# Kernel optimization log

Measured on AMD Instinct MI355X. Metric: run time of the kernel, lower is better.

The kernel has to match this reference:

```python
import jax, jax.numpy as jnp
import numpy as np

N_HEAD = 16
ROPE_BASE = 10000.0


def _make_rope(max_seq, half_dim):
    inv_freq = 1.0 / (ROPE_BASE ** (np.arange(0, half_dim, dtype=np.float32) / half_dim))
    t = np.arange(max_seq, dtype=np.float32)
    freqs = np.outer(t, inv_freq)  # [T, half_dim]
    return jnp.asarray(np.cos(freqs)), jnp.asarray(np.sin(freqs))


def setup_inputs() -> dict:
    key = jax.random.key(0)
    k1, k2, k3 = jax.random.split(key, 3)
    B, T, C = 4, 2048, 2048
    D = C // N_HEAD
    x = jax.random.normal(k1, (B, T, C), dtype=jnp.float32)
    # torch Linear weight [out,in]; stored transposed so y = x @ W
    wqkv = jax.random.normal(k2, (C, 3 * C), dtype=jnp.float32) * (C ** -0.5)
    wo = jax.random.normal(k3, (C, C), dtype=jnp.float32) * (C ** -0.5)
    rope_cos, rope_sin = _make_rope(T, D // 2)
    return {"x": x, "wqkv": wqkv, "wo": wo, "rope_cos": rope_cos, "rope_sin": rope_sin}


def _apply_rope(t, cos, sin):
    # t: [B, T, H, D]; cos/sin: [T, D/2]
    B, T, H, D = t.shape
    tr = t.reshape(B, T, H, D // 2, 2)
    xr, xi = tr[..., 0], tr[..., 1]
    c = cos[:T][None, :, None, :]
    s = sin[:T][None, :, None, :]
    out_r = xr * c - xi * s
    out_i = xr * s + xi * c
    return jnp.stack([out_r, out_i], axis=-1).reshape(B, T, H, D)


def reference(x, wqkv, wo, rope_cos, rope_sin):
    B, T, C = x.shape
    H = N_HEAD
    D = C // H
    qkv = x @ wqkv  # [B, T, 3C]
    q, k, v = jnp.split(qkv, 3, axis=-1)
    q = _apply_rope(q.reshape(B, T, H, D), rope_cos, rope_sin)
    k = _apply_rope(k.reshape(B, T, H, D), rope_cos, rope_sin)
    v = v.reshape(B, T, H, D)
    scale = D ** -0.5
    scores = jnp.einsum('bqhd,bkhd->bhqk', q, k) * scale  # [B, H, T, T]
    causal = jnp.tril(jnp.ones((T, T), dtype=bool))
    scores = jnp.where(causal[None, None], scores, jnp.finfo(scores.dtype).min)
    attn = jax.nn.softmax(scores, axis=-1)
    y = jnp.einsum('bhqk,bkhd->bqhd', attn, v).reshape(B, T, C)
    return y @ wo
```

## Files before the change

### kernel.cpp

```cpp
#include <hip/hip_runtime.h>
#include <hip/hip_bf16.h>

typedef __attribute__((ext_vector_type(8))) __bf16 bf16x8;
typedef __attribute__((ext_vector_type(4))) float f32x4;
typedef __attribute__((ext_vector_type(4))) unsigned short us4;

__device__ __forceinline__ unsigned short f2bf(float f) {
    unsigned u = __float_as_uint(f);
    u += 0x7FFFu + ((u >> 16) & 1u);
    return (unsigned short)(u >> 16);
}

__device__ __forceinline__ void gload16(const void* g, void* l) {
    __builtin_amdgcn_global_load_lds(
        (const __attribute__((address_space(1))) unsigned int*)g,
        (__attribute__((address_space(3))) unsigned int*)l,
        16, 0, 0);
}

__global__ void cvt_f32_bf16(const float* __restrict__ in, unsigned short* __restrict__ out, int n4) {
    int i = blockIdx.x * blockDim.x + threadIdx.x;
    if (i >= n4) return;
    float4 v = ((const float4*)in)[i];
    us4 r = { f2bf(v.x), f2bf(v.y), f2bf(v.z), f2bf(v.w) };
    ((us4*)out)[i] = r;
}

__global__ void tcvt(const float* __restrict__ in, unsigned short* __restrict__ out, int R, int C) {
    __shared__ float tile[32][33];
    int tx = threadIdx.x & 31, ty = threadIdx.x >> 5;
    int c0 = blockIdx.x * 32, r0 = blockIdx.y * 32;
    #pragma unroll
    for (int i = 0; i < 32; i += 8)
        tile[ty + i][tx] = in[(size_t)(r0 + ty + i) * C + c0 + tx];
    __syncthreads();
    #pragma unroll
    for (int i = 0; i < 32; i += 8)
        out[(size_t)(c0 + ty + i) * R + r0 + tx] = f2bf(tile[tx][ty + i]);
}

#define MFW(af, bf, fi, ni) acc[fi][ni] = __builtin_amdgcn_mfma_f32_16x16x32_bf16(af, bf, acc[fi][ni], 0, 0, 0)
#define MFMA16W() do { \
    MFW(a0,b0,0,0); MFW(a0,b1,0,1); MFW(a0,b2,0,2); MFW(a0,b3,0,3); \
    MFW(a1,b0,1,0); MFW(a1,b1,1,1); MFW(a1,b2,1,2); MFW(a1,b3,1,3); \
    MFW(a2,b0,2,0); MFW(a2,b1,2,1); MFW(a2,b2,2,2); MFW(a2,b3,2,3); \
    MFW(a3,b0,3,0); MFW(a3,b1,3,1); MFW(a3,b2,3,2); MFW(a3,b3,3,3); } while(0)
#define STGW(kt, bufo) do { \
    size_t ko = (size_t)(kt) * 128; \
    char* bb = L + (bufo); \
    gload16(Ag + sR + ko, bb + dstA); \
    gload16(Ag + sR2 + ko, bb + dstA + 16384); \
    gload16(Bg + sR + ko, bb + 32768 + dstA); \
    gload16(Bg + sR2 + ko, bb + 32768 + dstA + 16384); } while (0)

template <int MODE>
__global__ __launch_bounds__(1024, 4) void gemmw(
    const unsigned short* __restrict__ A, const unsigned short* __restrict__ Bt,
    int M, int N, int K, float* __restrict__ Cf,
    unsigned short* __restrict__ qp, unsigned short* __restrict__ kp,
    unsigned short* __restrict__ vTp,
    const float* __restrict__ ropeC, const float* __restrict__ ropeS,
    int cby, int cbx)
{
    __shared__ unsigned short lds[2][32768];
    const int tid = threadIdx.x;
    const int lane = tid & 63, wid = tid >> 6;
    const int ln15 = lane & 15, hig = lane >> 4;
    const int wrow = wid >> 2, wcol = wid & 3;

    int nwg = gridDim.x * gridDim.y;
    int flat = blockIdx.y * gridDim.x + blockIdx.x;
    int bx, by;
    if ((nwg & 7) == 0) {
        int c = flat & 7, local = flat >> 3;
        int chunkCols = gridDim.x / cbx;
        by = (c / chunkCols) * cby + local / cbx;
        bx = (c % chunkCols) * cbx + local % cbx;
    } else {
        bx = flat % gridDim.x; by = flat / gridDim.x;
    }
    const int mbase = by * 256, nbase = bx * 256;
    const size_t Kb = (size_t)K * 2;

    const char* Ag = (const char*)A + (size_t)mbase * Kb;
    const char* Bg = (const char*)Bt + (size_t)nbase * Kb;
    char* L = (char*)&lds[0][0];

    const int srow = tid >> 3;
    const int gs = (tid & 7) ^ (srow & 7);
    const size_t sR = (size_t)srow * Kb + gs * 16;
    const size_t sR2 = sR + (size_t)128 * Kb;
    const int dstA = tid * 16;

    const int aBase = (wrow * 64 + ln15) * 128;
    const int bBase = 32768 + (wcol * 64 + ln15) * 128;
    const int sl0 = (hig ^ (ln15 & 7)) * 16;
    const int sl1 = ((4 + hig) ^ (ln15 & 7)) * 16;

    f32x4 acc[4][4] = {};
    const int T = K >> 6;

    STGW(0, 0);
    asm volatile("s_waitcnt vmcnt(0)" ::: "memory");
    __builtin_amdgcn_s_barrier();
    asm volatile("" ::: "memory");

    for (int t = 0; t < T; t++) {
        char* bb = L + (t & 1) * 65536;
        if (t + 1 < T) STGW(t + 1, ((t + 1) & 1) * 65536);
        bf16x8 a0, a1, a2, a3, b0, b1, b2, b3;
        a0 = *(const bf16x8*)(bb + aBase + 0 * 2048 + sl0);
        a1 = *(const bf16x8*)(bb + aBase + 1 * 2048 + sl0);
        a2 = *(const bf16x8*)(bb + aBase + 2 * 2048 + sl0);
        a3 = *(const bf16x8*)(bb + aBase + 3 * 2048 + sl0);
        b0 = *(const bf16x8*)(bb + bBase + 0 * 2048 + sl0);
        b1 = *(const bf16x8*)(bb + bBase + 1 * 2048 + sl0);
        b2 = *(const bf16x8*)(bb + bBase + 2 * 2048 + sl0);
        b3 = *(const bf16x8*)(bb + bBase + 3 * 2048 + sl0);
        MFMA16W();
        a0 = *(const bf16x8*)(bb + aBase + 0 * 2048 + sl1);
        a1 = *(const bf16x8*)(bb + aBase + 1 * 2048 + sl1);
        a2 = *(const bf16x8*)(bb + aBase + 2 * 2048 + sl1);
        a3 = *(const bf16x8*)(bb + aBase + 3 * 2048 + sl1);
        b0 = *(const bf16x8*)(bb + bBase + 0 * 2048 + sl1);
        b1 = *(const bf16x8*)(bb + bBase + 1 * 2048 + sl1);
        b2 = *(const bf16x8*)(bb + bBase + 2 * 2048 + sl1);
        b3 = *(const bf16x8*)(bb + bBase + 3 * 2048 + sl1);
        MFMA16W();

        if (t + 1 < T) {
            asm volatile("s_waitcnt vmcnt(0)" ::: "memory");
            __builtin_amdgcn_s_barrier();
            asm volatile("" ::: "memory");
        }
    }

    if (MODE == 0) {
        #pragma unroll
        for (int fm = 0; fm < 4; fm++)
            #pragma unroll
            for (int fn = 0; fn < 4; fn++)
                #pragma unroll
                for (int j = 0; j < 4; j++) {
                    int m = mbase + wrow * 64 + fm * 16 + hig * 4 + j;
                    int col = nbase + wcol * 64 + fn * 16 + ln15;
                    Cf[(size_t)m * N + col] = acc[fm][fn][j];
                }
    } else {
        const int colb = nbase + wcol * 64;
        const int sec = colb >> 11;
        if (sec < 2) {
            unsigned short* dst = (sec == 0) ? qp : kp;
            const float scale = (sec == 0) ? 0.08838834764831845f : 1.0f;
            #pragma unroll
            for (int fm = 0; fm < 4; fm++)
                #pragma unroll
                for (int fn = 0; fn < 4; fn++) {
                    int within = (colb & 2047) + fn * 16 + ln15;
                    int h = within >> 7, d = within & 127, pidx = d >> 1;
                    #pragma unroll
                    for (int j = 0; j < 4; j++) {
                        int m = mbase + wrow * 64 + fm * 16 + hig * 4 + j;
                        int b = m >> 11, tq = m & 2047;
                        float v = acc[fm][fn][j];
                        float pv = __shfl_xor(v, 1);
                        float c = ropeC[tq * 64 + pidx], s = ropeS[tq * 64 + pidx];
                        float o = (d & 1) ? fmaf(pv, s, v * c) : fmaf(-pv, s, v * c);
                        o *= scale;
                        dst[((size_t)((b << 4) + h) * 2048 + tq) * 128 + d] = f2bf(o);
                    }
                }
        } else {
            #pragma unroll
            for (int fm = 0; fm < 4; fm++)
                #pragma unroll
                for (int fn = 0; fn < 4; fn++) {
                    int within = (colb & 2047) + fn * 16 + ln15;
                    int h = within >> 7, d = within & 127;
                    int m0 = mbase + wrow * 64 + fm * 16 + hig * 4;
                    int b = m0 >> 11, t0 = m0 & 2047;
                    us4 pk = { f2bf(acc[fm][fn][0]), f2bf(acc[fm][fn][1]),
                               f2bf(acc[fm][fn][2]), f2bf(acc[fm][fn][3]) };
                    *(us4*)(vTp + ((size_t)((b << 4) + h) * 128 + d) * 2048 + t0) = pk;
                }
        }
    }
}

__global__ __launch_bounds__(256, 2) void attn_fwd(
    const unsigned short* __restrict__ q, const unsigned short* __restrict__ k,
    const unsigned short* __restrict__ vT, unsigned short* __restrict__ outp)
{
    __shared__ unsigned short lK[2][64 * 128];
    __shared__ unsigned short lV[2][128 * 64];
    __shared__ unsigned short lP[4 * 32 * 64];
    const int tid = threadIdx.x;
    const int lane = tid & 63, wid = tid >> 6;
    const int ln15 = lane & 15, hig = lane >> 4, hi8 = hig * 8;
    const int bh = blockIdx.x;

    const char* qg = (const char*)(q + (size_t)bh * 2048 * 128);
    const char* kg = (const char*)(k + (size_t)bh * 2048 * 128);
    const char* vg = (const char*)(vT + (size_t)bh * 128 * 2048);
    char* lKc = (char*)&lK[0][0];
    char* lVc = (char*)&lV[0][0];
    char* lPc = (char*)lP + wid * (32 * 64 * 2);
    const int b = bh >> 4, h = bh & 15;

    for (int rep = 0; rep < 2; rep++) {
        const int qt = rep == 0 ? (int)blockIdx.y : 15 - (int)blockIdx.y;
        const int qbase = qt * 128;
        const int qw = qbase + wid * 32;

        bf16x8 qf[2][4];
        #pragma unroll
        for (int mt = 0; mt < 2; mt++)
            #pragma unroll
            for (int ks = 0; ks < 4; ks++)
                qf[mt][ks] = *(const bf16x8*)(qg + ((size_t)(qw + mt * 16 + ln15) * 128 + ks * 32 + hi8) * 2);

        f32x4 o[2][8] = {};
        float mreg[2] = { -1e30f, -1e30f };
        float lreg[2] = { 0.f, 0.f };

        auto stageKV = [&](int bf, int kv0) {
            #pragma unroll
            for (int i = 0; i < 4; i++) {
                int slot = tid + i * 256;
                int row = slot >> 4, c = (slot & 15) * 16;
                gload16(kg + (size_t)(kv0 + row) * 256 + (c ^ ((row & 7) << 4)),
                        lKc + bf * 16384 + slot * 16);
            }
            #pragma unroll
            for (int i = 0; i < 4; i++) {
                int slot = tid + i * 256;
                int d = slot >> 3, c = (slot & 7) * 16;
                gload16(vg + (size_t)d * 4096 + (size_t)kv0 * 2 + (c ^ ((d & 7) << 4)),
                        lVc + bf * 16384 + slot * 16);
            }
        };

        const int ntiles = (qbase >> 6) + 2;
        stageKV(0, 0);
        if (ntiles > 1) stageKV(1, 64);

        for (int it = 0; it < ntiles; it++) {
            const int kv0 = it * 64;
            const int buf = it & 1;
            if (it + 1 < ntiles) asm volatile("s_waitcnt vmcnt(8)" ::: "memory");
            else                 asm volatile("s_waitcnt vmcnt(0)" ::: "memory");
            __builtin_amdgcn_s_barrier();

            if (kv0 <= qw + 31) {
                const char* lKb = lKc + buf * 16384;
                const char* lVb = lVc + buf * 16384;

                f32x4 s[2][4] = {};
                #pragma unroll
                for (int ks = 0; ks < 4; ks++) {
                    bf16x8 kf[4];
                    #pragma unroll
                    for (int nt = 0; nt < 4; nt++) {
                        int row = nt * 16 + ln15;
                        kf[nt] = *(const bf16x8*)(lKb + row * 256 + (((ks * 32 + hi8) * 2) ^ ((row & 7) << 4)));
                    }
                    __builtin_amdgcn_s_setprio(1);
                    #pragma unroll
                    for (int mt = 0; mt < 2; mt++)
                        #pragma unroll
                        for (int nt = 0; nt < 4; nt++)
                            s[mt][nt] = __builtin_amdgcn_mfma_f32_16x16x32_bf16(kf[nt], qf[mt][ks], s[mt][nt], 0, 0, 0);
                    __builtin_amdgcn_s_setprio(0);
                }

                if (kv0 + 63 > qw) {
                    #pragma unroll
                    for (int mt = 0; mt < 2; mt++) {
                        int qi = qw + mt * 16 + ln15;
                        #pragma unroll
                        for (int nt = 0; nt < 4; nt++)
                            #pragma unroll
                            for (int j = 0; j < 4; j++) {
                                int kvi = kv0 + nt * 16 + 4 * hig + j;
                                if (kvi > qi) s[mt][nt][j] = -1e30f;
                            }
                    }
                }

                float vmax[2];
                #pragma unroll
                for (int mt = 0; mt < 2; mt++) {
                    float v = fmaxf(fmaxf(s[mt][0][0], s[mt][0][1]), fmaxf(s[mt][0][2], s[mt][0][3]));
                    #pragma unroll
                    for (int nt = 1; nt < 4; nt++)
                        v = fmaxf(v, fmaxf(fmaxf(s[mt][nt][0], s[mt][nt][1]), fmaxf(s[mt][nt][2], s[mt][nt][3])));
                    v = fmaxf(v, __shfl_xor(v, 16));
                    v = fmaxf(v, __shfl_xor(v, 32));
                    vmax[mt] = v;
                }
                bool grow = (vmax[0] > mreg[0] + 8.0f) || (vmax[1] > mreg[1] + 8.0f);
                if (__any(grow)) {
                    float sc[2];
                    #pragma unroll
                    for (int mt = 0; mt < 2; mt++) {
                        float mn = fmaxf(mreg[mt], vmax[mt]);
                        sc[mt] = __expf(mreg[mt] - mn);
                        mreg[mt] = mn;
                        lreg[mt] *= sc[mt];
                    }
                    #pragma unroll
                    for (int mt = 0; mt < 2; mt++)
                        #pragma unroll
                        for (int j = 0; j < 4; j++) {
                            float scj = __shfl(sc[mt], 4 * hig + j);
                            #pragma unroll
                            for (int ntd = 0; ntd < 8; ntd++) o[mt][ntd][j] *= scj;
                        }
                }
                #pragma unroll
                for (int mt = 0; mt < 2; mt++) {
                    float rs = 0.f;
                    #pragma unroll
                    for (int nt = 0; nt < 4; nt++)
                        #pragma unroll
                        for (int j = 0; j < 4; j++) {
                            float p = __expf(s[mt][nt][j] - mreg[mt]);
                            s[mt][nt][j] = p;
                            rs += p;
                        }
                    rs += __shfl_xor(rs, 16);
                    rs += __shfl_xor(rs, 32);
                    lreg[mt] += rs;
                }

                #pragma unroll
                for (int mt = 0; mt < 2; mt++) {
                    int rr = mt * 16 + ln15;
                    int rx = (rr & 7) << 4;
                    #pragma unroll
                    for (int nt = 0; nt < 4; nt++) {
                        us4 pk = { f2bf(s[mt][nt][0]), f2bf(s[mt][nt][1]),
                                   f2bf(s[mt][nt][2]), f2bf(s[mt][nt][3]) };
                        int addr = rr * 128 + ((nt * 32 + hig * 8) ^ rx);
                        *(us4*)(lPc + addr) = pk;
                    }
                }

                #pragma unroll
                for (int ks2 = 0; ks2 < 2; ks2++) {
                    bf16x8 pf[2];
                    #pragma unroll
                    for (int mt = 0; mt < 2; mt++) {
                        int row = mt * 16 + ln15;
                        pf[mt] = *(const bf16x8*)(lPc + row * 128 + (((ks2 * 32 + hi8) * 2) ^ ((row & 7) << 4)));
                    }
                    #pragma unroll
                    for (int ntd = 0; ntd < 8; ntd++) {
                        int drow = ntd * 16 + ln15;
                        bf16x8 vf = *(const bf16x8*)(lVb + drow * 128 + (((ks2 * 32 + hi8) * 2) ^ ((drow & 7) << 4)));
                        __builtin_amdgcn_s_setprio(1);
                        #pragma unroll
                        for (int mt = 0; mt < 2; mt++)
                            o[mt][ntd] = __builtin_amdgcn_mfma_f32_16x16x32_bf16(pf[mt], vf, o[mt][ntd], 0, 0, 0);
                        __builtin_amdgcn_s_setprio(0);
                    }
                }
            }

            __builtin_amdgcn_s_barrier();
            if (it + 2 < ntiles) stageKV(buf, kv0 + 128);
        }

        #pragma unroll
        for (int mt = 0; mt < 2; mt++)
            #pragma unroll
            for (int j = 0; j < 4; j++) {
                float inv = 1.0f / __shfl(lreg[mt], 4 * hig + j);
                int t = qw + mt * 16 + hig * 4 + j;
                #pragma unroll
                for (int ntd = 0; ntd < 8; ntd++) {
                    int d = ntd * 16 + ln15;
                    outp[((size_t)b * 2048 + t) * 2048 + h * 128 + d] = f2bf(o[mt][ntd][j] * inv);
                }
            }
    }
}

extern "C" void kernel_launch(void* const* d_in, const int* in_sizes, int n_in,
                              void* d_out, int out_size, void* d_ws, size_t ws_size,
                              hipStream_t stream) {
    const float* x     = (const float*)d_in[0];
    const float* wqkv  = (const float*)d_in[1];
    const float* wo    = (const float*)d_in[2];
    const float* ropeC = (const float*)d_in[3];
    const float* ropeS = (const float*)d_in[4];
    float* out = (float*)d_out;
    char* ws = (char*)d_ws;
    const size_t MB = 1024 * 1024;
    unsigned short* xb    = (unsigned short*)(ws);
    unsigned short* wqkvT = (unsigned short*)(ws + 32 * MB);
    unsigned short* woT   = (unsigned short*)(ws + 56 * MB);
    unsigned short* qb    = (unsigned short*)(ws + 64 * MB);
    unsigned short* kb    = (unsigned short*)(ws + 96 * MB);
    unsigned short* vTb   = (unsigned short*)(ws + 128 * MB);
    unsigned short* attnb = (unsigned short*)(ws + 160 * MB);

    cvt_f32_bf16<<<16384, 256, 0, stream>>>(x, xb, 4194304);
    tcvt<<<dim3(192, 64), 256, 0, stream>>>(wqkv, wqkvT, 2048, 6144);
    tcvt<<<dim3(64, 64), 256, 0, stream>>>(wo, woT, 2048, 2048);
    gemmw<1><<<dim3(24, 32), 1024, 0, stream>>>(xb, wqkvT, 8192, 6144, 2048,
                                                nullptr, qb, kb, vTb, ropeC, ropeS, 8, 12);
    attn_fwd<<<dim3(64, 8), 256, 0, stream>>>(qb, kb, vTb, attnb);
    gemmw<0><<<dim3(8, 32), 1024, 0, stream>>>(attnb, woT, 8192, 2048, 2048,
                                               out, nullptr, nullptr, nullptr, nullptr, nullptr, 4, 8);
}
```

Baseline: 401.5 us.

## Halve GEMM K-tile with paired-row LDS layout and narrow output-projection N tile

```diff
diff --git a/kernel.cpp b/kernel.cpp
--- a/kernel.cpp
+++ b/kernel.cpp
@@ -40,21 +40,9 @@
 }
 
 #define MFW(af, bf, fi, ni) acc[fi][ni] = __builtin_amdgcn_mfma_f32_16x16x32_bf16(af, bf, acc[fi][ni], 0, 0, 0)
-#define MFMA16W() do { \
-    MFW(a0,b0,0,0); MFW(a0,b1,0,1); MFW(a0,b2,0,2); MFW(a0,b3,0,3); \
-    MFW(a1,b0,1,0); MFW(a1,b1,1,1); MFW(a1,b2,1,2); MFW(a1,b3,1,3); \
-    MFW(a2,b0,2,0); MFW(a2,b1,2,1); MFW(a2,b2,2,2); MFW(a2,b3,2,3); \
-    MFW(a3,b0,3,0); MFW(a3,b1,3,1); MFW(a3,b2,3,2); MFW(a3,b3,3,3); } while(0)
-#define STGW(kt, bufo) do { \
-    size_t ko = (size_t)(kt) * 128; \
-    char* bb = L + (bufo); \
-    gload16(Ag + sR + ko, bb + dstA); \
-    gload16(Ag + sR2 + ko, bb + dstA + 16384); \
-    gload16(Bg + sR + ko, bb + 32768 + dstA); \
-    gload16(Bg + sR2 + ko, bb + 32768 + dstA + 16384); } while (0)
-
-template <int MODE>
-__global__ __launch_bounds__(1024, 4) void gemmw(
+
+template <int MODE, int BN>
+__global__ __launch_bounds__(1024) void gemmw(
     const unsigned short* __restrict__ A, const unsigned short* __restrict__ Bt,
     int M, int N, int K, float* __restrict__ Cf,
     unsigned short* __restrict__ qp, unsigned short* __restrict__ kp,
@@ -62,7 +50,11 @@
     const float* __restrict__ ropeC, const float* __restrict__ ropeS,
     int cby, int cbx)
 {
-    __shared__ unsigned short lds[2][32768];
+    constexpr int ASZ = 16384;
+    constexpr int BSZ = (BN >> 1) * 128;
+    constexpr int BUF = ASZ + BSZ;
+    constexpr int FN = BN / 64;
+    __shared__ char lds[2 * BUF];
     const int tid = threadIdx.x;
     const int lane = tid & 63, wid = tid >> 6;
     const int ln15 = lane & 15, hig = lane >> 4;
@@ -79,54 +71,57 @@
     } else {
         bx = flat % gridDim.x; by = flat / gridDim.x;
     }
-    const int mbase = by * 256, nbase = bx * 256;
+    const int mbase = by * 256, nbase = bx * BN;
     const size_t Kb = (size_t)K * 2;
 
     const char* Ag = (const char*)A + (size_t)mbase * Kb;
     const char* Bg = (const char*)Bt + (size_t)nbase * Kb;
-    char* L = (char*)&lds[0][0];
-
-    const int srow = tid >> 3;
-    const int gs = (tid & 7) ^ (srow & 7);
-    const size_t sR = (size_t)srow * Kb + gs * 16;
-    const size_t sR2 = sR + (size_t)128 * Kb;
-    const int dstA = tid * 16;
-
-    const int aBase = (wrow * 64 + ln15) * 128;
-    const int bBase = 32768 + (wcol * 64 + ln15) * 128;
-    const int sl0 = (hig ^ (ln15 & 7)) * 16;
-    const int sl1 = ((4 + hig) ^ (ln15 & 7)) * 16;
-
-    f32x4 acc[4][4] = {};
-    const int T = K >> 6;
-
-    STGW(0, 0);
+    char* L = (char*)lds;
+
+    const int ar = tid >> 3, as_ = tid & 7;
+    const int ac = as_ ^ (ar & 7);
+    const size_t aSrc = (size_t)(2 * ar + (ac >> 2)) * Kb + (ac & 3) * 16;
+    const int aDst = tid * 16;
+    const int bvalid = (BN == 256) || (tid < 512);
+    const int br = tid >> 3, bs_ = tid & 7;
+    const int bc = bs_ ^ (br & 7);
+    const size_t bSrc = (size_t)(2 * br + (bc >> 2)) * Kb + (bc & 3) * 16;
+    const int bDst = ASZ + tid * 16;
+
+    const int slotRW = (((ln15 & 1) << 2) | hig) ^ ((ln15 >> 1) & 7);
+    const int aOff = (wrow * 32 + (ln15 >> 1)) * 128 + slotRW * 16;
+    const int bOff = ASZ + ((BN == 256 ? wcol * 32 : wcol * 16) + (ln15 >> 1)) * 128 + slotRW * 16;
+
+    f32x4 acc[4][FN] = {};
+    const int T = K >> 5;
+
+    {
+        char* bb = L;
+        gload16(Ag + aSrc, bb + aDst);
+        if (bvalid) gload16(Bg + bSrc, bb + bDst);
+    }
     asm volatile("s_waitcnt vmcnt(0)" ::: "memory");
     __builtin_amdgcn_s_barrier();
     asm volatile("" ::: "memory");
 
     for (int t = 0; t < T; t++) {
-        char* bb = L + (t & 1) * 65536;
-        if (t + 1 < T) STGW(t + 1, ((t + 1) & 1) * 65536);
-        bf16x8 a0, a1, a2, a3, b0, b1, b2, b3;
-        a0 = *(const bf16x8*)(bb + aBase + 0 * 2048 + sl0);
-        a1 = *(const bf16x8*)(bb + aBase + 1 * 2048 + sl0);
-        a2 = *(const bf16x8*)(bb + aBase + 2 * 2048 + sl0);
-        a3 = *(const bf16x8*)(bb + aBase + 3 * 2048 + sl0);
-        b0 = *(const bf16x8*)(bb + bBase + 0 * 2048 + sl0);
-        b1 = *(const bf16x8*)(bb + bBase + 1 * 2048 + sl0);
-        b2 = *(const bf16x8*)(bb + bBase + 2 * 2048 + sl0);
-        b3 = *(const bf16x8*)(bb + bBase + 3 * 2048 + sl0);
-        MFMA16W();
-        a0 = *(const bf16x8*)(bb + aBase + 0 * 2048 + sl1);
-        a1 = *(const bf16x8*)(bb + aBase + 1 * 2048 + sl1);
-        a2 = *(const bf16x8*)(bb + aBase + 2 * 2048 + sl1);
-        a3 = *(const bf16x8*)(bb + aBase + 3 * 2048 + sl1);
-        b0 = *(const bf16x8*)(bb + bBase + 0 * 2048 + sl1);
-        b1 = *(const bf16x8*)(bb + bBase + 1 * 2048 + sl1);
-        b2 = *(const bf16x8*)(bb + bBase + 2 * 2048 + sl1);
-        b3 = *(const bf16x8*)(bb + bBase + 3 * 2048 + sl1);
-        MFMA16W();
+        char* bb = L + (t & 1) * BUF;
+        if (t + 1 < T) {
+            char* nb = L + ((t + 1) & 1) * BUF;
+            size_t ko = (size_t)(t + 1) * 64;
+            gload16(Ag + aSrc + ko, nb + aDst);
+            if (bvalid) gload16(Bg + bSrc + ko, nb + bDst);
+        }
+        bf16x8 av[4], bv[FN];
+        #pragma unroll
+        for (int i = 0; i < 4; i++) av[i] = *(const bf16x8*)(bb + aOff + i * 1024);
+        #pragma unroll
+        for (int j = 0; j < FN; j++) bv[j] = *(const bf16x8*)(bb + bOff + j * 1024);
+        #pragma unroll
+        for (int i = 0; i < 4; i++)
+            #pragma unroll
+            for (int j = 0; j < FN; j++)
+                MFW(av[i], bv[j], i, j);
 
         if (t + 1 < T) {
             asm volatile("s_waitcnt vmcnt(0)" ::: "memory");
@@ -139,11 +134,11 @@
         #pragma unroll
         for (int fm = 0; fm < 4; fm++)
             #pragma unroll
-            for (int fn = 0; fn < 4; fn++)
+            for (int fn = 0; fn < FN; fn++)
                 #pragma unroll
                 for (int j = 0; j < 4; j++) {
                     int m = mbase + wrow * 64 + fm * 16 + hig * 4 + j;
-                    int col = nbase + wcol * 64 + fn * 16 + ln15;
+                    int col = nbase + wcol * (BN / 4) + fn * 16 + ln15;
                     Cf[(size_t)m * N + col] = acc[fm][fn][j];
                 }
     } else {
@@ -155,7 +150,7 @@
             #pragma unroll
             for (int fm = 0; fm < 4; fm++)
                 #pragma unroll
-                for (int fn = 0; fn < 4; fn++) {
+                for (int fn = 0; fn < FN; fn++) {
                     int within = (colb & 2047) + fn * 16 + ln15;
                     int h = within >> 7, d = within & 127, pidx = d >> 1;
                     #pragma unroll
@@ -174,7 +169,7 @@
             #pragma unroll
             for (int fm = 0; fm < 4; fm++)
                 #pragma unroll
-                for (int fn = 0; fn < 4; fn++) {
+                for (int fn = 0; fn < FN; fn++) {
                     int within = (colb & 2047) + fn * 16 + ln15;
                     int h = within >> 7, d = within & 127;
                     int m0 = mbase + wrow * 64 + fm * 16 + hig * 4;
@@ -408,9 +403,9 @@
     cvt_f32_bf16<<<16384, 256, 0, stream>>>(x, xb, 4194304);
     tcvt<<<dim3(192, 64), 256, 0, stream>>>(wqkv, wqkvT, 2048, 6144);
     tcvt<<<dim3(64, 64), 256, 0, stream>>>(wo, woT, 2048, 2048);
-    gemmw<1><<<dim3(24, 32), 1024, 0, stream>>>(xb, wqkvT, 8192, 6144, 2048,
-                                                nullptr, qb, kb, vTb, ropeC, ropeS, 8, 12);
+    gemmw<1, 256><<<dim3(24, 32), 1024, 0, stream>>>(xb, wqkvT, 8192, 6144, 2048,
+                                                     nullptr, qb, kb, vTb, ropeC, ropeS, 8, 12);
     attn_fwd<<<dim3(64, 8), 256, 0, stream>>>(qb, kb, vTb, attnb);
-    gemmw<0><<<dim3(8, 32), 1024, 0, stream>>>(attnb, woT, 8192, 2048, 2048,
-                                               out, nullptr, nullptr, nullptr, nullptr, nullptr, 4, 8);
-}
+    gemmw<0, 128><<<dim3(16, 32), 1024, 0, stream>>>(attnb, woT, 8192, 2048, 2048,
+                                                     out, nullptr, nullptr, nullptr, nullptr, nullptr, 8, 8);
+}
```

After: 429.0 us. +6.9%, slower.
